# Kernel optimization log

Measured on AMD Instinct MI355X. Metric: run time of the kernel, lower is better.

## Reference

```python
import jax, jax.numpy as jnp
import numpy as np

B, S, H, E = 64, 512, 1024, 10  # batch, encoder seq len, hidden, n_events
LSTM_IN = H + 1 + E  # context (H) + x (1) + sim_scores (E)


def setup_inputs() -> dict:
    key = jax.random.key(0)
    ks = jax.random.split(key, 20)
    s = 0.02
    return {
        "x": jax.random.normal(ks[0], (B, 1), jnp.float32),
        "h0": jax.random.normal(ks[1], (1, B, H), jnp.float32),
        "c0": jax.random.normal(ks[2], (1, B, H), jnp.float32),
        "encoder_output": jax.random.normal(ks[3], (B, S, H), jnp.float32),
        "W_enc": jax.random.normal(ks[4], (H, H), jnp.float32) * s,
        "W_dec": jax.random.normal(ks[5], (H, H), jnp.float32) * s,
        "w_val": jax.random.normal(ks[6], (H,), jnp.float32) * s,
        "W_gate": jax.random.normal(ks[7], (E, E), jnp.float32) * s,
        "events_mat": jax.random.normal(ks[8], (E, H), jnp.float32) * s,
        "W_ih": jax.random.normal(ks[9], (4 * H, LSTM_IN), jnp.float32) * s,
        "W_hh": jax.random.normal(ks[10], (4 * H, H), jnp.float32) * s,
        "b_ih": jax.random.normal(ks[11], (4 * H,), jnp.float32) * s,
        "b_hh": jax.random.normal(ks[12], (4 * H,), jnp.float32) * s,
        "ln_g": jnp.ones((H,), jnp.float32),
        "ln_b": jnp.zeros((H,), jnp.float32),
        "W_fin": jax.random.normal(ks[13], (1, H), jnp.float32) * s,
        "b_fin": jnp.zeros((1,), jnp.float32),
    }


def reference(x, h0, c0, encoder_output, W_enc, W_dec, w_val, W_gate,
              events_mat, W_ih, W_hh, b_ih, b_hh, ln_g, ln_b, W_fin, b_fin):
    h = h0[0]  # [B,H] (num_layers == 1)
    c = c0[0]
    # Bahdanau attention: v^T tanh(W_e enc + W_d h)
    proj = jnp.einsum('bsh,gh->bsg', encoder_output, W_enc) + (h @ W_dec.T)[:, None, :]
    attn_scores = jnp.tanh(proj) @ w_val  # [B,S]
    attn_weight = jax.nn.softmax(attn_scores, axis=1)
    context = jnp.einsum('bs,bsh->bh', attn_weight, encoder_output)  # [B,H]
    # event similarity + gate
    sim_scores = (context @ events_mat.T) @ W_gate.T  # [B,E]
    # single-step LSTM on concat(context, sim, x)
    xin = jnp.concatenate([context, sim_scores, x], axis=1)  # [B, H+E+1]
    gates = xin @ W_ih.T + b_ih + h @ W_hh.T + b_hh  # [B,4H]
    i, f, g, o = jnp.split(gates, 4, axis=1)  # torch gate order: i,f,g,o
    c_new = jax.nn.sigmoid(f) * c + jax.nn.sigmoid(i) * jnp.tanh(g)
    h_new = jax.nn.sigmoid(o) * jnp.tanh(c_new)  # [B,H]
    # LayerNorm(eps=1e-5)
    mu = jnp.mean(h_new, axis=-1, keepdims=True)
    var = jnp.mean(jnp.square(h_new - mu), axis=-1, keepdims=True)
    y = (h_new - mu) / jnp.sqrt(var + 1e-5) * ln_g + ln_b
    fin_output = y @ W_fin.T + b_fin  # [B,1]
    return fin_output, (h_new[None], c_new[None]), attn_weight, sim_scores
```

## Files before the change

### kernel.cpp

```cpp
#include <hip/hip_runtime.h>
#include <math.h>

#define Bn 64
#define Sn 512
#define Hn 1024
#define En 10
#define Mn (Bn*Sn)
#define KIN 1035
#define KP  2112

#define OUT_FIN 0
#define OUT_H   64
#define OUT_C   65600
#define OUT_AW  131136
#define OUT_SIM 163904

#define WS_ENCB  0
#define WS_WENCB 16777216
#define WS_WTS   17301504
#define WS_PART  17334272
#define WS_CTXP  17334272
#define WS_WDECB 17858560
#define WS_H0B   18382848
#define WS_DPART 18415616
#define WS_WCATB 0
#define WS_GPART 4325376
#define WS_XINB  6422528

typedef __attribute__((ext_vector_type(8))) short bf16x8;
typedef __attribute__((ext_vector_type(4))) float f32x4;

#define ASYNC_CP16(gptr, lptr) \
  __builtin_amdgcn_global_load_lds((const __attribute__((address_space(1))) void*)(gptr), \
                                   (__attribute__((address_space(3))) void*)(lptr), 16, 0, 0)

static __device__ __forceinline__ unsigned short f2bf(float f) {
    union { float f; unsigned int u; } v; v.f = f;
    unsigned int r = (v.u + 0x7fffu + ((v.u >> 16) & 1u)) >> 16;
    return (unsigned short)r;
}
static __device__ __forceinline__ float bf2f(unsigned short h) {
    union { unsigned int u; float f; } v; v.u = ((unsigned int)h) << 16;
    return v.f;
}
static __device__ __forceinline__ float fast_tanh(float x) {
    float cx = fminf(15.f, fmaxf(-15.f, x));
    float e = __expf(2.f * cx);
    return (e - 1.f) * __builtin_amdgcn_rcpf(e + 1.f);
}

__global__ __launch_bounds__(256) void k_cast(const float* __restrict__ enc,
                                              const float* __restrict__ Wenc,
                                              const float* __restrict__ Wdec,
                                              const float* __restrict__ h0,
                                              unsigned short* __restrict__ encB,
                                              unsigned short* __restrict__ wencB,
                                              unsigned short* __restrict__ wdecB,
                                              unsigned short* __restrict__ h0B) {
    int bid = blockIdx.x;
    const float* src; unsigned short* dst; size_t off;
    if (bid < 16384)      { src = enc;  dst = encB;  off = (size_t)bid * 2048; }
    else if (bid < 16896) { src = Wenc; dst = wencB; off = (size_t)(bid - 16384) * 2048; }
    else if (bid < 17408) { src = Wdec; dst = wdecB; off = (size_t)(bid - 16896) * 2048; }
    else                  { src = h0;   dst = h0B;   off = (size_t)(bid - 17408) * 2048; }
    off += (size_t)threadIdx.x * 8;
    float4 v0 = *(const float4*)(src + off);
    float4 v1 = *(const float4*)(src + off + 4);
    ushort4 a; a.x = f2bf(v0.x); a.y = f2bf(v0.y); a.z = f2bf(v0.z); a.w = f2bf(v0.w);
    ushort4 b; b.x = f2bf(v1.x); b.y = f2bf(v1.y); b.z = f2bf(v1.z); b.w = f2bf(v1.w);
    *(ushort4*)(dst + off)     = a;
    *(ushort4*)(dst + off + 4) = b;
}

__global__ __launch_bounds__(256) void k1_gemm(const unsigned short* __restrict__ h0B,
                                               const unsigned short* __restrict__ wdecB,
                                               float* __restrict__ dpart) {
    __shared__ short As[4096];
    __shared__ short Bs[8192];

    const int n0 = blockIdx.x * 128;
    const int sp = blockIdx.y;
    const int kbeg = sp * 128;
    const int tid  = threadIdx.x;
    const int wave = tid >> 6;
    const int lane = tid & 63;
    const int wr = wave >> 1;
    const int wc = wave & 1;
    const int q4 = lane >> 4;
    const int ml = lane & 15;

    f32x4 acc[2][4];
#pragma unroll
    for (int i = 0; i < 2; ++i)
#pragma unroll
        for (int j = 0; j < 4; ++j) acc[i][j] = (f32x4){0.f, 0.f, 0.f, 0.f};

    const unsigned short* bTile = wdecB + (size_t)n0 * 1024;

    for (int kk = 0; kk < 2; ++kk) {
        int k0 = kbeg + kk * 64;
        __syncthreads();
#pragma unroll
        for (int t = 0; t < 2; ++t) {
            int q = wave * 2 + t;
            ASYNC_CP16(h0B + (size_t)lane * 1024 + k0 + q * 8, &As[(q * 64) * 8]);
        }
#pragma unroll
        for (int t = 0; t < 4; ++t) {
            int cb = t * 4 + wave;
            int q  = cb >> 1;
            int mb = (cb & 1) << 6;
            ASYNC_CP16(bTile + (size_t)(mb + lane) * 1024 + k0 + q * 8,
                       &Bs[(q * 128 + mb) * 8]);
        }
        __syncthreads();
#pragma unroll
        for (int s = 0; s < 2; ++s) {
            bf16x8 af[2], bfr[4];
#pragma unroll
            for (int i = 0; i < 2; ++i)
                af[i] = *(const bf16x8*)&As[((((s << 2) + q4) * 64) + wr * 32 + (i << 4) + ml) * 8];
#pragma unroll
            for (int j = 0; j < 4; ++j)
                bfr[j] = *(const bf16x8*)&Bs[((((s << 2) + q4) * 128) + wc * 64 + (j << 4) + ml) * 8];
#pragma unroll
            for (int i = 0; i < 2; ++i)
#pragma unroll
                for (int j = 0; j < 4; ++j)
                    acc[i][j] = __builtin_amdgcn_mfma_f32_16x16x32_bf16(af[i], bfr[j], acc[i][j], 0, 0, 0);
        }
    }
#pragma unroll
    for (int i = 0; i < 2; ++i)
#pragma unroll
        for (int j = 0; j < 4; ++j)
#pragma unroll
            for (int r = 0; r < 4; ++r) {
                int m = wr * 32 + (i << 4) + q4 * 4 + r;
                int n = n0 + wc * 64 + (j << 4) + ml;
                dpart[((size_t)sp * 64 + m) * 1024 + n] = acc[i][j][r];
            }
}

__global__ __launch_bounds__(512, 4) void k2_scores(const unsigned short* __restrict__ encB,
                                                    const unsigned short* __restrict__ wencB,
                                                    const float* __restrict__ dpart,
                                                    const float* __restrict__ wval,
                                                    float* __restrict__ part) {
    __shared__ short As[16384];
    __shared__ short Bs[16384];

    const int bid = blockIdx.x;
    const int m0 = (bid >> 3) * 128;
    const int nb = bid & 7;
    const int n0 = nb * 128;
    const int b  = m0 >> 9;
    const int tid  = threadIdx.x;
    const int wave = tid >> 6;
    const int lane = tid & 63;
    const int wr = wave >> 1;
    const int wc = wave & 1;
    const int q4 = lane >> 4;
    const int ml = lane & 15;

    f32x4 acc[2][4];
#pragma unroll
    for (int i = 0; i < 2; ++i)
#pragma unroll
        for (int j = 0; j < 4; ++j) acc[i][j] = (f32x4){0.f, 0.f, 0.f, 0.f};

    const unsigned short* aTile = encB  + (size_t)m0 * 1024;
    const unsigned short* bTile = wencB + (size_t)n0 * 1024;

    for (int k0 = 0; k0 < 1024; k0 += 128) {
        __syncthreads();
#pragma unroll
        for (int t = 0; t < 8; ++t) {
            int c = t * 8 + wave;
            if (c < 32) {
                int q  = c >> 1;
                int mb = (c & 1) << 6;
                ASYNC_CP16(aTile + (size_t)(mb + lane) * 1024 + k0 + q * 8,
                           &As[(q * 128 + mb) * 8]);
            } else {
                int c2 = c - 32;
                int q  = c2 >> 1;
                int mb = (c2 & 1) << 6;
                ASYNC_CP16(bTile + (size_t)(mb + lane) * 1024 + k0 + q * 8,
                           &Bs[(q * 128 + mb) * 8]);
            }
        }
        __syncthreads();
#pragma unroll
        for (int s = 0; s < 4; ++s) {
            bf16x8 af[2], bfr[4];
            int q = (s << 2) + q4;
#pragma unroll
            for (int i = 0; i < 2; ++i)
                af[i] = *(const bf16x8*)&As[((q * 128) + wr * 32 + (i << 4) + ml) * 8];
#pragma unroll
            for (int j = 0; j < 4; ++j)
                bfr[j] = *(const bf16x8*)&Bs[((q * 128) + wc * 64 + (j << 4) + ml) * 8];
#pragma unroll
            for (int i = 0; i < 2; ++i)
#pragma unroll
                for (int j = 0; j < 4; ++j)
                    acc[i][j] = __builtin_amdgcn_mfma_f32_16x16x32_bf16(af[i], bfr[j], acc[i][j], 0, 0, 0);
        }
    }

    float dpv[4], wvv[4];
#pragma unroll
    for (int j = 0; j < 4; ++j) {
        int n = n0 + wc * 64 + (j << 4) + ml;
        float d = 0.f;
#pragma unroll
        for (int sp = 0; sp < 8; ++sp) d += dpart[((size_t)sp * 64 + b) * 1024 + n];
        dpv[j] = d;
        wvv[j] = wval[n];
    }
    __syncthreads();
    float* rsum = (float*)As;
#pragma unroll
    for (int i = 0; i < 2; ++i) {
#pragma unroll
        for (int r = 0; r < 4; ++r) {
            float p = 0.f;
#pragma unroll
            for (int j = 0; j < 4; ++j) p += fast_tanh(acc[i][j][r] + dpv[j]) * wvv[j];
            p += __shfl_xor(p, 1);
            p += __shfl_xor(p, 2);
            p += __shfl_xor(p, 4);
            p += __shfl_xor(p, 8);
            if (ml == 0) rsum[wc * 128 + wr * 32 + (i << 4) + q4 * 4 + r] = p;
        }
    }
    __syncthreads();
    if (tid < 128)
        part[(size_t)nb * Mn + m0 + tid] = rsum[tid] + rsum[128 + tid];
}

__device__ __forceinline__ float block_sum256(float v, float* red, int tid) {
#pragma unroll
    for (int off = 1; off < 64; off <<= 1) v += __shfl_xor(v, off);
    if ((tid & 63) == 0) red[tid >> 6] = v;
    __syncthreads();
    v = red[0] + red[1] + red[2] + red[3];
    __syncthreads();
    return v;
}

__global__ __launch_bounds__(256) void k3a_softmax(const float* __restrict__ part,
                                                   float* __restrict__ wts,
                                                   float* __restrict__ out) {
    int b = blockIdx.x;
    int tid = threadIdx.x;
    __shared__ float red[8];
    int s0 = tid, s1 = tid + 256;
    float v0 = 0.f, v1 = 0.f;
#pragma unroll
    for (int nb = 0; nb < 8; ++nb) {
        v0 += part[(size_t)nb * Mn + b * 512 + s0];
        v1 += part[(size_t)nb * Mn + b * 512 + s1];
    }
    float mx = fmaxf(v0, v1);
#pragma unroll
    for (int off = 1; off < 64; off <<= 1) mx = fmaxf(mx, __shfl_xor(mx, off));
    if ((tid & 63) == 0) red[tid >> 6] = mx;
    __syncthreads();
    mx = fmaxf(fmaxf(red[0], red[1]), fmaxf(red[2], red[3]));
    __syncthreads();
    float e0 = __expf(v0 - mx), e1 = __expf(v1 - mx);
    float sm = block_sum256(e0 + e1, red, tid);
    float inv = 1.0f / sm;
    float w0 = e0 * inv, w1 = e1 * inv;
    wts[b * 512 + s0] = w0;
    wts[b * 512 + s1] = w1;
    out[OUT_AW + b * 512 + s0] = w0;
    out[OUT_AW + b * 512 + s1] = w1;
}

__global__ __launch_bounds__(256) void k3b_context(const unsigned short* __restrict__ encB,
                                                   const float* __restrict__ wts,
                                                   float* __restrict__ ctxp) {
    int b  = blockIdx.y;
    int sc = blockIdx.x >> 1;
    int hh = blockIdx.x & 1;
    int h2 = (hh * 256 + threadIdx.x) * 2;
    const unsigned short* e = encB + (size_t)b * Sn * Hn + (size_t)sc * 64 * Hn + h2;
    const float* w = wts + b * 512 + sc * 64;
    float a0 = 0.f, a1 = 0.f, b0 = 0.f, b1 = 0.f;
    for (int s = 0; s < 64; s += 2) {
        unsigned int p0 = *(const unsigned int*)(e + (size_t)(s + 0) * 1024);
        unsigned int p1 = *(const unsigned int*)(e + (size_t)(s + 1) * 1024);
        a0 += w[s + 0] * bf2f((unsigned short)(p0 & 0xffffu));
        b0 += w[s + 0] * bf2f((unsigned short)(p0 >> 16));
        a1 += w[s + 1] * bf2f((unsigned short)(p1 & 0xffffu));
        b1 += w[s + 1] * bf2f((unsigned short)(p1 >> 16));
    }
    ctxp[((size_t)sc * 64 + b) * 1024 + h2]     = a0 + a1;
    ctxp[((size_t)sc * 64 + b) * 1024 + h2 + 1] = b0 + b1;
}

__global__ __launch_bounds__(256) void k4_sim(const float* __restrict__ ctxp,
                                              const float* __restrict__ events,
                                              const float* __restrict__ Wg,
                                              float* __restrict__ out) {
    int b = blockIdx.x;
    int tid = threadIdx.x, wv = tid >> 6, lane = tid & 63;
    __shared__ float cl[1024];
    __shared__ float tmp[16];
#pragma unroll
    for (int i = 0; i < 4; ++i) {
        int h = tid + i * 256;
        float v = 0.f;
#pragma unroll
        for (int sc = 0; sc < 8; ++sc) v += ctxp[((size_t)sc * 64 + b) * 1024 + h];
        cl[h] = v;
    }
    __syncthreads();
    for (int e = wv; e < 10; e += 4) {
        const float* ev = events + e * 1024;
        float a = 0.f;
#pragma unroll
        for (int kk = 0; kk < 1024; kk += 64) a += cl[kk + lane] * ev[kk + lane];
#pragma unroll
        for (int off = 1; off < 64; off <<= 1) a += __shfl_xor(a, off);
        if (lane == 0) tmp[e] = a;
    }
    __syncthreads();
    if (tid < 10) {
        float s2 = 0.f;
#pragma unroll
        for (int e = 0; e < 10; ++e) s2 += Wg[tid * 10 + e] * tmp[e];
        out[OUT_SIM + b * 10 + tid] = s2;
    }
}

__global__ __launch_bounds__(256) void k_castW(const float* __restrict__ Wih,
                                               const float* __restrict__ Whh,
                                               unsigned short* __restrict__ WcatB) {
    unsigned int idx = blockIdx.x * 256 + threadIdx.x;
    unsigned int r = idx / KP;
    unsigned int k = idx - r * KP;
    float v = 0.f;
    if (k < 1035)      v = Wih[(size_t)r * 1035 + k];
    else if (k < 2059) v = Whh[(size_t)r * 1024 + (k - 1035)];
    WcatB[idx] = f2bf(v);
}

__global__ __launch_bounds__(256) void k_xinB(const float* __restrict__ ctxp,
                                              const float* __restrict__ simOut,
                                              const float* __restrict__ x,
                                              const float* __restrict__ h0,
                                              unsigned short* __restrict__ xinB) {
    unsigned int idx = blockIdx.x * 256 + threadIdx.x;
    unsigned int b = idx / KP;
    unsigned int k = idx - b * KP;
    float v = 0.f;
    if (k < 1024) {
        v = 0.f;
#pragma unroll
        for (int sc = 0; sc < 8; ++sc) v += ctxp[((size_t)sc * 64 + b) * 1024 + k];
    }
    else if (k < 1034)  v = simOut[b * 10 + (k - 1024)];
    else if (k == 1034) v = x[b];
    else if (k < 2059)  v = h0[b * 1024 + (k - 1035)];
    xinB[idx] = f2bf(v);
}

__global__ __launch_bounds__(256) void k5_gemm(const unsigned short* __restrict__ xinB,
                                               const unsigned short* __restrict__ WcatB,
                                               float* __restrict__ gpart) {
    __shared__ short As[4096];
    __shared__ short Bs[8192];

    const int n0 = blockIdx.x * 128;
    const int sp = blockIdx.y;
    const int kbeg   = (sp == 0) ? 0 : (5 + (sp - 1) * 4) * 64;
    const int ksteps = (sp == 0) ? 5 : 4;
    const int tid  = threadIdx.x;
    const int wave = tid >> 6;
    const int lane = tid & 63;
    const int wr = wave >> 1;
    const int wc = wave & 1;
    const int q4 = lane >> 4;
    const int ml = lane & 15;

    f32x4 acc[2][4];
#pragma unroll
    for (int i = 0; i < 2; ++i)
#pragma unroll
        for (int j = 0; j < 4; ++j) acc[i][j] = (f32x4){0.f, 0.f, 0.f, 0.f};

    const unsigned short* bTile = WcatB + (size_t)n0 * KP;

    for (int kk = 0; kk < ksteps; ++kk) {
        int k0 = kbeg + kk * 64;
        __syncthreads();
#pragma unroll
        for (int t = 0; t < 2; ++t) {
            int q = wave * 2 + t;
            ASYNC_CP16(xinB + (size_t)lane * KP + k0 + q * 8, &As[(q * 64) * 8]);
        }
#pragma unroll
        for (int t = 0; t < 4; ++t) {
            int cb = t * 4 + wave;
            int q  = cb >> 1;
            int mb = (cb & 1) << 6;
            ASYNC_CP16(bTile + (size_t)(mb + lane) * KP + k0 + q * 8,
                       &Bs[(q * 128 + mb) * 8]);
        }
        __syncthreads();
#pragma unroll
        for (int s = 0; s < 2; ++s) {
            bf16x8 af[2], bfr[4];
#pragma unroll
            for (int i = 0; i < 2; ++i)
                af[i] = *(const bf16x8*)&As[((((s << 2) + q4) * 64) + wr * 32 + (i << 4) + ml) * 8];
#pragma unroll
            for (int j = 0; j < 4; ++j)
                bfr[j] = *(const bf16x8*)&Bs[((((s << 2) + q4) * 128) + wc * 64 + (j << 4) + ml) * 8];
#pragma unroll
            for (int i = 0; i < 2; ++i)
#pragma unroll
                for (int j = 0; j < 4; ++j)
                    acc[i][j] = __builtin_amdgcn_mfma_f32_16x16x32_bf16(af[i], bfr[j], acc[i][j], 0, 0, 0);
        }
    }
#pragma unroll
    for (int i = 0; i < 2; ++i)
#pragma unroll
        for (int j = 0; j < 4; ++j)
#pragma unroll
            for (int r = 0; r < 4; ++r) {
                int m = wr * 32 + (i << 4) + q4 * 4 + r;
                int n = n0 + wc * 64 + (j << 4) + ml;
                gpart[((size_t)sp * 64 + m) * 4096 + n] = acc[i][j][r];
            }
}

__global__ __launch_bounds__(256) void k56_lstm_ln(const float* __restrict__ gpart,
                                                   const float* __restrict__ bih,
                                                   const float* __restrict__ bhh,
                                                   const float* __restrict__ c0,
                                                   const float* __restrict__ lng,
                                                   const float* __restrict__ lnb,
                                                   const float* __restrict__ Wfin,
                                                   const float* __restrict__ bfin,
                                                   float* __restrict__ out) {
    int b = blockIdx.x, tid = threadIdx.x;
    __shared__ float red[8];
    float hn[4];
#pragma unroll
    for (int r = 0; r < 4; ++r) {
        int u = tid + (r << 8);
        float g[4];
#pragma unroll
        for (int gt = 0; gt < 4; ++gt) {
            int rr = gt * 1024 + u;
            float a = bih[rr] + bhh[rr];
#pragma unroll
            for (int sp = 0; sp < 8; ++sp)
                a += gpart[((size_t)sp * 64 + b) * 4096 + rr];
            g[gt] = a;
        }
        float cp = c0[b * 1024 + u];
        float si = 1.f / (1.f + __expf(-g[0]));
        float sf = 1.f / (1.f + __expf(-g[1]));
        float so = 1.f / (1.f + __expf(-g[3]));
        float cn = sf * cp + si * tanhf(g[2]);
        hn[r] = so * tanhf(cn);
        out[OUT_H + b * 1024 + u] = hn[r];
        out[OUT_C + b * 1024 + u] = cn;
    }
    float mu = block_sum256(hn[0] + hn[1] + hn[2] + hn[3], red, tid) * (1.f / 1024.f);
    float d0 = hn[0] - mu, d1 = hn[1] - mu, d2 = hn[2] - mu, d3 = hn[3] - mu;
    float var = block_sum256(d0 * d0 + d1 * d1 + d2 * d2 + d3 * d3, red, tid) * (1.f / 1024.f);
    float rstd = rsqrtf(var + 1e-5f);
    float acc = (d0 * rstd * lng[tid]       + lnb[tid])       * Wfin[tid]
              + (d1 * rstd * lng[tid + 256] + lnb[tid + 256]) * Wfin[tid + 256]
              + (d2 * rstd * lng[tid + 512] + lnb[tid + 512]) * Wfin[tid + 512]
              + (d3 * rstd * lng[tid + 768] + lnb[tid + 768]) * Wfin[tid + 768];
    acc = block_sum256(acc, red, tid);
    if (tid == 0) out[OUT_FIN + b] = acc + bfin[0];
}

extern "C" void kernel_launch(void* const* d_in, const int* in_sizes, int n_in,
                              void* d_out, int out_size, void* d_ws, size_t ws_size,
                              hipStream_t stream) {
    (void)in_sizes; (void)n_in; (void)out_size; (void)ws_size;
    const float* x    = (const float*)d_in[0];
    const float* h0   = (const float*)d_in[1];
    const float* c0   = (const float*)d_in[2];
    const float* enc  = (const float*)d_in[3];
    const float* Wenc = (const float*)d_in[4];
    const float* Wdec = (const float*)d_in[5];
    const float* wval = (const float*)d_in[6];
    const float* Wg   = (const float*)d_in[7];
    const float* ev   = (const float*)d_in[8];
    const float* Wih  = (const float*)d_in[9];
    const float* Whh  = (const float*)d_in[10];
    const float* bih  = (const float*)d_in[11];
    const float* bhh  = (const float*)d_in[12];
    const float* lng  = (const float*)d_in[13];
    const float* lnb  = (const float*)d_in[14];
    const float* Wfin = (const float*)d_in[15];
    const float* bfin = (const float*)d_in[16];

    float* out  = (float*)d_out;
    float* ws   = (float*)d_ws;
    unsigned short* encB  = (unsigned short*)(ws + WS_ENCB);
    unsigned short* wencB = (unsigned short*)(ws + WS_WENCB);
    unsigned short* wdecB = (unsigned short*)(ws + WS_WDECB);
    unsigned short* h0B   = (unsigned short*)(ws + WS_H0B);
    float* dpart = ws + WS_DPART;
    float* wts   = ws + WS_WTS;
    float* part  = ws + WS_PART;
    float* ctxp  = ws + WS_CTXP;
    unsigned short* WcatB = (unsigned short*)(ws + WS_WCATB);
    float* gpart = ws + WS_GPART;
    unsigned short* xinB  = (unsigned short*)(ws + WS_XINB);

    k_cast     <<<17440, 256, 0, stream>>>(enc, Wenc, Wdec, h0, encB, wencB, wdecB, h0B);
    k1_gemm    <<<dim3(8, 8), 256, 0, stream>>>(h0B, wdecB, dpart);
    k2_scores  <<<2048, 512, 0, stream>>>(encB, wencB, dpart, wval, part);
    k3a_softmax<<<64, 256, 0, stream>>>(part, wts, out);
    k3b_context<<<dim3(16, 64), 256, 0, stream>>>(encB, wts, ctxp);
    k4_sim     <<<64, 256, 0, stream>>>(ctxp, ev, Wg, out);
    k_castW    <<<33792, 256, 0, stream>>>(Wih, Whh, WcatB);
    k_xinB     <<<528, 256, 0, stream>>>(ctxp, out + OUT_SIM, x, h0, xinB);
    k5_gemm    <<<dim3(32, 8), 256, 0, stream>>>(xinB, WcatB, gpart);
    k56_lstm_ln<<<64, 256, 0, stream>>>(gpart, bih, bhh, c0, lng, lnb, Wfin, bfin, out);
}
```

Baseline: 462.8 us.

## Shrink score GEMM tiles, fuse xin build into sim kernel, 2D castW grid

The attention-score GEMM now uses 64x128 tiles with 256-thread blocks and a K step of 64. That is twice as many blocks with less LDS each, aiming for higher occupancy. The xin bf16 packing is folded into the sim kernel, which reuses the context already reduced in LDS and removes one launch and the second 8-way ctxp reduction. The weight cast kernel uses a 2D grid, which removes the per-thread integer division. Smaller tiles lower operand reuse in the dominant GEMM, and the fused kernel runs only 64 blocks for the xin writes.

```diff
diff --git a/kernel.cpp b/kernel.cpp
--- a/kernel.cpp
+++ b/kernel.cpp
@@ -142,16 +142,16 @@
             }
 }
 
-__global__ __launch_bounds__(512, 4) void k2_scores(const unsigned short* __restrict__ encB,
+__global__ __launch_bounds__(256, 5) void k2_scores(const unsigned short* __restrict__ encB,
                                                     const unsigned short* __restrict__ wencB,
                                                     const float* __restrict__ dpart,
                                                     const float* __restrict__ wval,
                                                     float* __restrict__ part) {
-    __shared__ short As[16384];
-    __shared__ short Bs[16384];
+    __shared__ short As[4096];
+    __shared__ short Bs[8192];
 
     const int bid = blockIdx.x;
-    const int m0 = (bid >> 3) * 128;
+    const int m0 = (bid >> 3) * 64;
     const int nb = bid & 7;
     const int n0 = nb * 128;
     const int b  = m0 >> 9;
@@ -172,35 +172,31 @@
     const unsigned short* aTile = encB  + (size_t)m0 * 1024;
     const unsigned short* bTile = wencB + (size_t)n0 * 1024;
 
-    for (int k0 = 0; k0 < 1024; k0 += 128) {
+    for (int k0 = 0; k0 < 1024; k0 += 64) {
         __syncthreads();
 #pragma unroll
-        for (int t = 0; t < 8; ++t) {
-            int c = t * 8 + wave;
-            if (c < 32) {
-                int q  = c >> 1;
-                int mb = (c & 1) << 6;
-                ASYNC_CP16(aTile + (size_t)(mb + lane) * 1024 + k0 + q * 8,
-                           &As[(q * 128 + mb) * 8]);
-            } else {
-                int c2 = c - 32;
-                int q  = c2 >> 1;
-                int mb = (c2 & 1) << 6;
-                ASYNC_CP16(bTile + (size_t)(mb + lane) * 1024 + k0 + q * 8,
-                           &Bs[(q * 128 + mb) * 8]);
-            }
+        for (int t = 0; t < 2; ++t) {
+            int q = wave * 2 + t;
+            ASYNC_CP16(aTile + (size_t)lane * 1024 + k0 + q * 8, &As[(q * 64) * 8]);
+        }
+#pragma unroll
+        for (int t = 0; t < 4; ++t) {
+            int cb = t * 4 + wave;
+            int q  = cb >> 1;
+            int mb = (cb & 1) << 6;
+            ASYNC_CP16(bTile + (size_t)(mb + lane) * 1024 + k0 + q * 8,
+                       &Bs[(q * 128 + mb) * 8]);
         }
         __syncthreads();
 #pragma unroll
-        for (int s = 0; s < 4; ++s) {
+        for (int s = 0; s < 2; ++s) {
             bf16x8 af[2], bfr[4];
-            int q = (s << 2) + q4;
 #pragma unroll
             for (int i = 0; i < 2; ++i)
-                af[i] = *(const bf16x8*)&As[((q * 128) + wr * 32 + (i << 4) + ml) * 8];
+                af[i] = *(const bf16x8*)&As[((((s << 2) + q4) * 64) + wr * 32 + (i << 4) + ml) * 8];
 #pragma unroll
             for (int j = 0; j < 4; ++j)
-                bfr[j] = *(const bf16x8*)&Bs[((q * 128) + wc * 64 + (j << 4) + ml) * 8];
+                bfr[j] = *(const bf16x8*)&Bs[((((s << 2) + q4) * 128) + wc * 64 + (j << 4) + ml) * 8];
 #pragma unroll
             for (int i = 0; i < 2; ++i)
 #pragma unroll
@@ -232,12 +228,12 @@
             p += __shfl_xor(p, 2);
             p += __shfl_xor(p, 4);
             p += __shfl_xor(p, 8);
-            if (ml == 0) rsum[wc * 128 + wr * 32 + (i << 4) + q4 * 4 + r] = p;
-        }
-    }
-    __syncthreads();
-    if (tid < 128)
-        part[(size_t)nb * Mn + m0 + tid] = rsum[tid] + rsum[128 + tid];
+            if (ml == 0) rsum[wc * 64 + wr * 32 + (i << 4) + q4 * 4 + r] = p;
+        }
+    }
+    __syncthreads();
+    if (tid < 64)
+        part[(size_t)nb * Mn + m0 + tid] = rsum[tid] + rsum[64 + tid];
 }
 
 __device__ __forceinline__ float block_sum256(float v, float* red, int tid) {
@@ -302,10 +298,13 @@
     ctxp[((size_t)sc * 64 + b) * 1024 + h2 + 1] = b0 + b1;
 }
 
-__global__ __launch_bounds__(256) void k4_sim(const float* __restrict__ ctxp,
-                                              const float* __restrict__ events,
-                                              const float* __restrict__ Wg,
-                                              float* __restrict__ out) {
+__global__ __launch_bounds__(256) void k4x_sim_xin(const float* __restrict__ ctxp,
+                                                   const float* __restrict__ events,
+                                                   const float* __restrict__ Wg,
+                                                   const float* __restrict__ x,
+                                                   const float* __restrict__ h0,
+                                                   float* __restrict__ out,
+                                                   unsigned short* __restrict__ xinB) {
     int b = blockIdx.x;
     int tid = threadIdx.x, wv = tid >> 6, lane = tid & 63;
     __shared__ float cl[1024];
@@ -329,44 +328,38 @@
         if (lane == 0) tmp[e] = a;
     }
     __syncthreads();
+    float sims[10];
+#pragma unroll
+    for (int e2 = 0; e2 < 10; ++e2) sims[e2] = tmp[e2];
     if (tid < 10) {
         float s2 = 0.f;
 #pragma unroll
-        for (int e = 0; e < 10; ++e) s2 += Wg[tid * 10 + e] * tmp[e];
+        for (int e = 0; e < 10; ++e) s2 += Wg[tid * 10 + e] * sims[e];
         out[OUT_SIM + b * 10 + tid] = s2;
+        tmp[tid] = s2;
+    }
+    __syncthreads();
+    for (int k = tid; k < KP; k += 256) {
+        float v;
+        if (k < 1024)       v = cl[k];
+        else if (k < 1034)  v = tmp[k - 1024];
+        else if (k == 1034) v = x[b];
+        else if (k < 2059)  v = h0[b * 1024 + (k - 1035)];
+        else                v = 0.f;
+        xinB[(size_t)b * KP + k] = f2bf(v);
     }
 }
 
 __global__ __launch_bounds__(256) void k_castW(const float* __restrict__ Wih,
                                                const float* __restrict__ Whh,
                                                unsigned short* __restrict__ WcatB) {
-    unsigned int idx = blockIdx.x * 256 + threadIdx.x;
-    unsigned int r = idx / KP;
-    unsigned int k = idx - r * KP;
+    unsigned int r = blockIdx.y;
+    unsigned int k = blockIdx.x * 256 + threadIdx.x;
+    if (k >= KP) return;
     float v = 0.f;
     if (k < 1035)      v = Wih[(size_t)r * 1035 + k];
     else if (k < 2059) v = Whh[(size_t)r * 1024 + (k - 1035)];
-    WcatB[idx] = f2bf(v);
-}
-
-__global__ __launch_bounds__(256) void k_xinB(const float* __restrict__ ctxp,
-                                              const float* __restrict__ simOut,
-                                              const float* __restrict__ x,
-                                              const float* __restrict__ h0,
-                                              unsigned short* __restrict__ xinB) {
-    unsigned int idx = blockIdx.x * 256 + threadIdx.x;
-    unsigned int b = idx / KP;
-    unsigned int k = idx - b * KP;
-    float v = 0.f;
-    if (k < 1024) {
-        v = 0.f;
-#pragma unroll
-        for (int sc = 0; sc < 8; ++sc) v += ctxp[((size_t)sc * 64 + b) * 1024 + k];
-    }
-    else if (k < 1034)  v = simOut[b * 10 + (k - 1024)];
-    else if (k == 1034) v = x[b];
-    else if (k < 2059)  v = h0[b * 1024 + (k - 1035)];
-    xinB[idx] = f2bf(v);
+    WcatB[(size_t)r * KP + k] = f2bf(v);
 }
 
 __global__ __launch_bounds__(256) void k5_gemm(const unsigned short* __restrict__ xinB,
@@ -524,12 +517,11 @@
 
     k_cast     <<<17440, 256, 0, stream>>>(enc, Wenc, Wdec, h0, encB, wencB, wdecB, h0B);
     k1_gemm    <<<dim3(8, 8), 256, 0, stream>>>(h0B, wdecB, dpart);
-    k2_scores  <<<2048, 512, 0, stream>>>(encB, wencB, dpart, wval, part);
+    k2_scores  <<<4096, 256, 0, stream>>>(encB, wencB, dpart, wval, part);
     k3a_softmax<<<64, 256, 0, stream>>>(part, wts, out);
     k3b_context<<<dim3(16, 64), 256, 0, stream>>>(encB, wts, ctxp);
-    k4_sim     <<<64, 256, 0, stream>>>(ctxp, ev, Wg, out);
-    k_castW    <<<33792, 256, 0, stream>>>(Wih, Whh, WcatB);
-    k_xinB     <<<528, 256, 0, stream>>>(ctxp, out + OUT_SIM, x, h0, xinB);
+    k4x_sim_xin<<<64, 256, 0, stream>>>(ctxp, ev, Wg, x, h0, out, xinB);
+    k_castW    <<<dim3(9, 4096), 256, 0, stream>>>(Wih, Whh, WcatB);
     k5_gemm    <<<dim3(32, 8), 256, 0, stream>>>(xinB, WcatB, gpart);
     k56_lstm_ln<<<64, 256, 0, stream>>>(gpart, bih, bhh, c0, lng, lnb, Wfin, bfin, out);
 }
```

Result: slower. 505.3 us (+9.2%).
